# Optimization experiments

Measured on AMD Instinct MI355X. Metric: run time of the kernel, lower is better.

## Reference

```python
import jax, jax.numpy as jnp
import numpy as np

B, NN, HL = 64, 64, 50
IN_DIM, POS_DIM, ATT_DIM = 384, 64, 256
NEWS_DIM = IN_DIM + POS_DIM  # 448


def setup_inputs() -> dict:
    key = jax.random.key(0)
    ks = jax.random.split(key, 8)
    pos_emb = jax.random.uniform(ks[3], (100, POS_DIM), jnp.float32, -0.1, 0.1)
    pos_emb = pos_emb.at[0].set(0.0)  # initialize() zeros row 0
    return {
        "log_vec": jax.random.normal(ks[0], (B, HL, IN_DIM), jnp.float32),
        "log_mask": jax.random.randint(ks[1], (B, HL), 0, 2, jnp.int32),
        "news_vec": jax.random.normal(ks[2], (B, NN, IN_DIM), jnp.float32),
        "pos_emb": pos_emb,
        "W1": jax.random.normal(ks[4], (ATT_DIM, 2 * NEWS_DIM), jnp.float32) * 0.02,
        "b1": jnp.zeros((ATT_DIM,), jnp.float32),
        "W2": jax.random.normal(ks[5], (1, ATT_DIM), jnp.float32) * 0.02,
        "b2": jnp.zeros((1,), jnp.float32),
    }


def reference(log_vec, log_mask, news_vec, pos_emb, W1, b1, W2, b2):
    b, nn_ = news_vec.shape[:2]
    hl = log_mask.shape[1]
    # append position embeddings (row 0 for candidates, rows 1..hl for history)
    nf = jnp.concatenate(
        [news_vec, jnp.broadcast_to(pos_emb[0], (b, nn_, POS_DIM))], axis=-1)   # (B,NN,ND)
    lf = jnp.concatenate(
        [log_vec, jnp.broadcast_to(pos_emb[1:hl + 1], (b, hl, POS_DIM))], axis=-1)  # (B,HL,ND)
    # affine1(cat[news, log]) == news @ Wn^T + log @ Wl^T + b1 (avoids concat)
    Wn, Wl = W1[:, :NEWS_DIM], W1[:, NEWS_DIM:]
    pn = jnp.einsum('bnd,ad->bna', nf, Wn)   # (B,NN,A)
    pl = jnp.einsum('bhd,ad->bha', lf, Wl)   # (B,HL,A)
    h = jnp.tanh(pn[:, :, None, :] + pl[:, None, :, :] + b1)  # (B,NN,HL,A)
    logits = jnp.einsum('bnha,a->bnh', h, W2[0]) + b2[0]      # (B,NN,HL)
    logits = jnp.where(log_mask[:, None, :] == 0, jnp.float32(-1e9), logits)
    attn = jax.nn.softmax(logits, axis=2)
    user_log_vecs = jnp.einsum('bnh,bhd->bnd', attn, lf)      # (B,NN,ND)
    return user_log_vecs, nf
```

## Files before the change

kernel.cpp:

```cpp
#include <hip/hip_runtime.h>
#include <math.h>

typedef unsigned short u16;
typedef unsigned int   u32;

#define B_       64
#define NN_      64
#define HL_      50
#define IN_DIM   384
#define POS_DIM  64
#define ATT_DIM  256
#define NEWS_DIM 448

typedef __attribute__((ext_vector_type(8))) short short8;
typedef __attribute__((ext_vector_type(4))) float f32x4;

#if __has_builtin(__builtin_amdgcn_exp2f)
#define EXP2F(x) __builtin_amdgcn_exp2f(x)
#else
#define EXP2F(x) exp2f(x)
#endif
#if __has_builtin(__builtin_amdgcn_rcpf)
#define RCPF(x) __builtin_amdgcn_rcpf(x)
#else
#define RCPF(x) (1.0f/(x))
#endif

__device__ __forceinline__ u16 f2bf(float f) {
    union { float f; u32 i; } v; v.f = f;
    u32 r = v.i + 0x7fffu + ((v.i >> 16) & 1u);
    return (u16)(r >> 16);
}
__device__ __forceinline__ float bf2f(u16 u) {
    union { u32 i; float f; } v; v.i = ((u32)u) << 16; return v.f;
}
__device__ __forceinline__ uint2 pack4(float4 v) {
    return make_uint2((u32)f2bf(v.x) | ((u32)f2bf(v.y) << 16),
                      (u32)f2bf(v.z) | ((u32)f2bf(v.w) << 16));
}
__device__ __forceinline__ float fast_tanh(float x) {
    float e = EXP2F(x * 2.88539008f);
    return 1.0f - 2.0f * RCPF(1.0f + e);
}

#define C_W   57344u
#define C_NV  393216u
#define C_LG  307200u
#define C_PS  51200u
#define C_NZ  65536u
#define C_TOT (C_W + C_NV + C_LG + C_PS + C_NZ)

__global__ __launch_bounds__(256) void prep_k(
    const float* __restrict__ W1, const float* __restrict__ newsv,
    const float* __restrict__ logv, const float* __restrict__ pos,
    u16* __restrict__ Wbf, u16* __restrict__ nv_bf, u16* __restrict__ lf_bf,
    float* __restrict__ nf)
{
    u32 i = blockIdx.x * 256u + threadIdx.x;
    if (i < C_W) {
        float4 v = *(const float4*)(W1 + (size_t)i * 4u);
        *(uint2*)(Wbf + (size_t)i * 4u) = pack4(v);
        return;
    }
    i -= C_W;
    if (i < C_NV) {
        float4 v = *(const float4*)(newsv + (size_t)i * 4u);
        *(uint2*)(nv_bf + (size_t)i * 4u) = pack4(v);
        u32 e = i * 4u, r = e / IN_DIM, d = e - r * IN_DIM;
        *(float4*)(nf + (size_t)r * NEWS_DIM + d) = v;
        return;
    }
    i -= C_NV;
    if (i < C_LG) {
        float4 v = *(const float4*)(logv + (size_t)i * 4u);
        u32 e = i * 4u, r = e / IN_DIM, d = e - r * IN_DIM;
        *(uint2*)(lf_bf + (size_t)r * NEWS_DIM + d) = pack4(v);
        return;
    }
    i -= C_LG;
    if (i < C_PS) {
        u32 e = i * 4u, r = e / POS_DIM, d = e - r * POS_DIM;
        u32 h = r % HL_;
        float4 v = *(const float4*)(pos + (size_t)(1u + h) * POS_DIM + d);
        *(uint2*)(lf_bf + (size_t)r * NEWS_DIM + IN_DIM + d) = pack4(v);
        return;
    }
    i -= C_PS;
    if (i < C_NZ) {
        u32 e = i * 4u, r = e / POS_DIM, d = e - r * POS_DIM;
        *(float4*)(nf + (size_t)r * NEWS_DIM + IN_DIM + d) = make_float4(0.f, 0.f, 0.f, 0.f);
    }
}

__global__ __launch_bounds__(64) void gemm_k(
    const u16* __restrict__ nv_bf, const u16* __restrict__ lf_bf,
    const u16* __restrict__ Wbf, const float* __restrict__ b1,
    float* __restrict__ pn, float* __restrict__ plT)
{
    int bid = blockIdx.x;
    int lane = threadIdx.x;
    int m = lane & 15, q = lane >> 4;
    bool is_pn = bid < 256;
    int r0, c0, lda, koff, klen;
    const u16* A;
    if (is_pn) { r0 = (bid & 63) * 64;       c0 = (bid >> 6) * 64; A = nv_bf; lda = IN_DIM;   koff = 0;        klen = IN_DIM; }
    else { int b2 = bid - 256; r0 = (b2 % 50) * 64; c0 = (b2 / 50) * 64; A = lf_bf; lda = NEWS_DIM; koff = NEWS_DIM; klen = NEWS_DIM; }

    f32x4 acc[4][4];
#pragma unroll
    for (int a = 0; a < 4; a++)
#pragma unroll
        for (int b = 0; b < 4; b++) acc[a][b] = (f32x4){0.f, 0.f, 0.f, 0.f};

    const u16* Ap = A + (size_t)(r0 + m) * lda + q * 8;
    const u16* Wp = Wbf + (size_t)(c0 + m) * (2 * NEWS_DIM) + koff + q * 8;

    for (int k = 0; k < klen; k += 32) {
        short8 af[4], wf[4];
#pragma unroll
        for (int rt = 0; rt < 4; rt++) af[rt] = *(const short8*)(Ap + rt * 16 * lda + k);
#pragma unroll
        for (int ct = 0; ct < 4; ct++) wf[ct] = *(const short8*)(Wp + ct * 16 * (2 * NEWS_DIM) + k);
#pragma unroll
        for (int rt = 0; rt < 4; rt++)
#pragma unroll
            for (int ct = 0; ct < 4; ct++)
                acc[rt][ct] = __builtin_amdgcn_mfma_f32_16x16x32_bf16(
                    af[rt], wf[ct], acc[rt][ct], 0, 0, 0);
    }
#pragma unroll
    for (int rt = 0; rt < 4; rt++)
#pragma unroll
        for (int ct = 0; ct < 4; ct++)
#pragma unroll
            for (int i = 0; i < 4; i++) {
                int gr = r0 + rt * 16 + q * 4 + i;
                int gc = c0 + ct * 16 + m;
                float v = acc[rt][ct][i];
                if (is_pn) {
                    pn[(size_t)gr * ATT_DIM + gc] = v + b1[gc];
                } else {
                    int bb = gr / HL_, hh = gr - bb * HL_;
                    plT[(size_t)(bb * ATT_DIM + gc) * HL_ + hh] = v;
                }
            }
}

__global__ __launch_bounds__(256) void attn_out_k(
    const float* __restrict__ pn, const float* __restrict__ plT,
    const float* __restrict__ w2, const int* __restrict__ lmask,
    const u16* __restrict__ lf_bf, float* __restrict__ out)
{
    __shared__ float at_s[4][64];
    int lane = threadIdx.x & 63;
    int wid = (int)(threadIdx.x >> 6);
    int g = blockIdx.x * 4 + wid;
    int b = g >> 6;
    int n = g & 63;
    int hl = (lane < HL_) ? lane : (HL_ - 1);
    const float* pr = pn + (size_t)g * ATT_DIM;
    const float* pl = plT + (size_t)b * ATT_DIM * HL_ + hl;

    float a0 = 0.f, a1 = 0.f, a2 = 0.f, a3 = 0.f;
#pragma unroll 4
    for (int a = 0; a < ATT_DIM; a += 4) {
        float4 w4 = *(const float4*)(w2 + a);
        float4 p  = *(const float4*)(pr + a);
        float l0 = pl[(a + 0) * HL_];
        float l1 = pl[(a + 1) * HL_];
        float l2 = pl[(a + 2) * HL_];
        float l3 = pl[(a + 3) * HL_];
        a0 = __builtin_fmaf(fast_tanh(p.x + l0), w4.x, a0);
        a1 = __builtin_fmaf(fast_tanh(p.y + l1), w4.y, a1);
        a2 = __builtin_fmaf(fast_tanh(p.z + l2), w4.z, a2);
        a3 = __builtin_fmaf(fast_tanh(p.w + l3), w4.w, a3);
    }
    float acc = (a0 + a1) + (a2 + a3);
    int mv = (lane < HL_) ? lmask[b * HL_ + lane] : 0;
    float logit = mv ? acc : -1e9f;
    float mx = logit;
#pragma unroll
    for (int o = 32; o > 0; o >>= 1) mx = fmaxf(mx, __shfl_xor(mx, o));
    float e = EXP2F((logit - mx) * 1.44269504f);
    float s = e;
#pragma unroll
    for (int o = 32; o > 0; o >>= 1) s += __shfl_xor(s, o);
    at_s[wid][lane] = e * RCPF(s);

    const u16* lfb = lf_bf + (size_t)b * HL_ * NEWS_DIM + lane;
    float acc7[7];
#pragma unroll
    for (int j = 0; j < 7; j++) acc7[j] = 0.f;
    for (int h = 0; h < HL_; h++) {
        float av = at_s[wid][h];
        const u16* row = lfb + (size_t)h * NEWS_DIM;
#pragma unroll
        for (int j = 0; j < 7; j++)
            acc7[j] = fmaf(av, bf2f(row[64 * j]), acc7[j]);
    }
    float* o0 = out + (size_t)g * NEWS_DIM + lane;
#pragma unroll
    for (int j = 0; j < 7; j++) o0[64 * j] = acc7[j];
}

extern "C" void kernel_launch(void* const* d_in, const int* in_sizes, int n_in,
                              void* d_out, int out_size, void* d_ws, size_t ws_size,
                              hipStream_t stream) {
    const float* logv  = (const float*)d_in[0];
    const int*   lmask = (const int*)d_in[1];
    const float* newsv = (const float*)d_in[2];
    const float* pos   = (const float*)d_in[3];
    const float* W1    = (const float*)d_in[4];
    const float* b1    = (const float*)d_in[5];
    const float* w2    = (const float*)d_in[6];

    float* out = (float*)d_out;
    float* nf  = out + (size_t)B_ * NN_ * NEWS_DIM;

    char* ws = (char*)d_ws;
    u16*   lf_bf = (u16*)(ws + 0);
    u16*   Wbf   = (u16*)(ws + 2867200);
    u16*   nv_bf = (u16*)(ws + 3325952);
    float* pn    = (float*)(ws + 6471680);
    float* plT   = (float*)(ws + 10665984);

    prep_k    <<<C_TOT / 256, 256, 0, stream>>>(W1, newsv, logv, pos,
                                                Wbf, nv_bf, lf_bf, nf);
    gemm_k    <<<456, 64, 0, stream>>>(nv_bf, lf_bf, Wbf, b1, pn, plT);
    attn_out_k<<<1024, 256, 0, stream>>>(pn, plT, w2, lmask, lf_bf, out);
}
```

Measured before the change: 133.2 us.

## Split GEMM into smaller tiles and attention over two waves per query

The GEMM tile shrinks from 64x64 to 16x64 per wave, raising the block count from 456 to 1824 so more of the GPU is busy, at the cost of less A/W reuse per wave. The attention kernel now gives each (b,n) query to two waves. Each wave takes half of the ATT_DIM reduction, the partial logits are combined through shared memory with a block barrier, and the two waves split the 448-wide output (one writes columns 0..255, the other 256..447, with a 64-column overlap that is computed twice but written once). This doubles the wave-level parallelism and shortens the serial tanh loop, but adds a __syncthreads and repeats the softmax and mask work in both waves.

Result: slower. 276.6 us (+107.6%).

```diff
diff --git a/kernel.cpp b/kernel.cpp
--- a/kernel.cpp
+++ b/kernel.cpp
@@ -100,71 +100,67 @@
     int bid = blockIdx.x;
     int lane = threadIdx.x;
     int m = lane & 15, q = lane >> 4;
-    bool is_pn = bid < 256;
+    bool is_pn = bid < 1024;
     int r0, c0, lda, koff, klen;
     const u16* A;
-    if (is_pn) { r0 = (bid & 63) * 64;       c0 = (bid >> 6) * 64; A = nv_bf; lda = IN_DIM;   koff = 0;        klen = IN_DIM; }
-    else { int b2 = bid - 256; r0 = (b2 % 50) * 64; c0 = (b2 / 50) * 64; A = lf_bf; lda = NEWS_DIM; koff = NEWS_DIM; klen = NEWS_DIM; }
-
-    f32x4 acc[4][4];
-#pragma unroll
-    for (int a = 0; a < 4; a++)
-#pragma unroll
-        for (int b = 0; b < 4; b++) acc[a][b] = (f32x4){0.f, 0.f, 0.f, 0.f};
+    if (is_pn) { r0 = (bid >> 2) * 16;  c0 = (bid & 3) * 64; A = nv_bf; lda = IN_DIM;   koff = 0;        klen = IN_DIM; }
+    else { int b2 = bid - 1024; r0 = (b2 >> 2) * 16; c0 = (b2 & 3) * 64; A = lf_bf; lda = NEWS_DIM; koff = NEWS_DIM; klen = NEWS_DIM; }
+
+    f32x4 acc[4];
+#pragma unroll
+    for (int b = 0; b < 4; b++) acc[b] = (f32x4){0.f, 0.f, 0.f, 0.f};
 
     const u16* Ap = A + (size_t)(r0 + m) * lda + q * 8;
     const u16* Wp = Wbf + (size_t)(c0 + m) * (2 * NEWS_DIM) + koff + q * 8;
 
     for (int k = 0; k < klen; k += 32) {
-        short8 af[4], wf[4];
-#pragma unroll
-        for (int rt = 0; rt < 4; rt++) af[rt] = *(const short8*)(Ap + rt * 16 * lda + k);
+        short8 af, wf[4];
+        af = *(const short8*)(Ap + k);
 #pragma unroll
         for (int ct = 0; ct < 4; ct++) wf[ct] = *(const short8*)(Wp + ct * 16 * (2 * NEWS_DIM) + k);
 #pragma unroll
-        for (int rt = 0; rt < 4; rt++)
-#pragma unroll
-            for (int ct = 0; ct < 4; ct++)
-                acc[rt][ct] = __builtin_amdgcn_mfma_f32_16x16x32_bf16(
-                    af[rt], wf[ct], acc[rt][ct], 0, 0, 0);
-    }
-#pragma unroll
-    for (int rt = 0; rt < 4; rt++)
-#pragma unroll
         for (int ct = 0; ct < 4; ct++)
-#pragma unroll
-            for (int i = 0; i < 4; i++) {
-                int gr = r0 + rt * 16 + q * 4 + i;
-                int gc = c0 + ct * 16 + m;
-                float v = acc[rt][ct][i];
-                if (is_pn) {
-                    pn[(size_t)gr * ATT_DIM + gc] = v + b1[gc];
-                } else {
-                    int bb = gr / HL_, hh = gr - bb * HL_;
-                    plT[(size_t)(bb * ATT_DIM + gc) * HL_ + hh] = v;
-                }
+            acc[ct] = __builtin_amdgcn_mfma_f32_16x16x32_bf16(af, wf[ct], acc[ct], 0, 0, 0);
+    }
+#pragma unroll
+    for (int ct = 0; ct < 4; ct++)
+#pragma unroll
+        for (int i = 0; i < 4; i++) {
+            int gr = r0 + q * 4 + i;
+            int gc = c0 + ct * 16 + m;
+            float v = acc[ct][i];
+            if (is_pn) {
+                pn[(size_t)gr * ATT_DIM + gc] = v + b1[gc];
+            } else {
+                int bb = gr / HL_, hh = gr - bb * HL_;
+                plT[(size_t)(bb * ATT_DIM + gc) * HL_ + hh] = v;
             }
-}
-
-__global__ __launch_bounds__(256) void attn_out_k(
+        }
+}
+
+__global__ __launch_bounds__(256, 8) void attn_out_k(
     const float* __restrict__ pn, const float* __restrict__ plT,
     const float* __restrict__ w2, const int* __restrict__ lmask,
     const u16* __restrict__ lf_bf, float* __restrict__ out)
 {
+    __shared__ float part[4][64];
     __shared__ float at_s[4][64];
     int lane = threadIdx.x & 63;
-    int wid = (int)(threadIdx.x >> 6);
-    int g = blockIdx.x * 4 + wid;
+    int wid = __builtin_amdgcn_readfirstlane((int)(threadIdx.x >> 6));
+    int pair = wid >> 1;
+    int half = wid & 1;
+    int g = blockIdx.x * 2 + pair;
     int b = g >> 6;
-    int n = g & 63;
     int hl = (lane < HL_) ? lane : (HL_ - 1);
-    const float* pr = pn + (size_t)g * ATT_DIM;
-    const float* pl = plT + (size_t)b * ATT_DIM * HL_ + hl;
+    int aoff = half * 128;
+    const float* pr = pn + (size_t)g * ATT_DIM + aoff;
+    const float* pl = plT + ((size_t)b * ATT_DIM + aoff) * HL_ + hl;
+    const float* w2o = w2 + aoff;
 
     float a0 = 0.f, a1 = 0.f, a2 = 0.f, a3 = 0.f;
-#pragma unroll 4
-    for (int a = 0; a < ATT_DIM; a += 4) {
-        float4 w4 = *(const float4*)(w2 + a);
+#pragma unroll 2
+    for (int a = 0; a < 128; a += 4) {
+        float4 w4 = *(const float4*)(w2o + a);
         float4 p  = *(const float4*)(pr + a);
         float l0 = pl[(a + 0) * HL_];
         float l1 = pl[(a + 1) * HL_];
@@ -176,6 +172,10 @@
         a3 = __builtin_fmaf(fast_tanh(p.w + l3), w4.w, a3);
     }
     float acc = (a0 + a1) + (a2 + a3);
+    part[wid][lane] = acc;
+    __syncthreads();
+    acc += part[wid ^ 1][lane];
+
     int mv = (lane < HL_) ? lmask[b * HL_ + lane] : 0;
     float logit = mv ? acc : -1e9f;
     float mx = logit;
@@ -187,20 +187,22 @@
     for (int o = 32; o > 0; o >>= 1) s += __shfl_xor(s, o);
     at_s[wid][lane] = e * RCPF(s);
 
-    const u16* lfb = lf_bf + (size_t)b * HL_ * NEWS_DIM + lane;
-    float acc7[7];
-#pragma unroll
-    for (int j = 0; j < 7; j++) acc7[j] = 0.f;
+    const u16* lfb = lf_bf + (size_t)b * HL_ * NEWS_DIM + half * 192 + lane;
+    float acc4[4];
+#pragma unroll
+    for (int j = 0; j < 4; j++) acc4[j] = 0.f;
     for (int h = 0; h < HL_; h++) {
         float av = at_s[wid][h];
         const u16* row = lfb + (size_t)h * NEWS_DIM;
 #pragma unroll
-        for (int j = 0; j < 7; j++)
-            acc7[j] = fmaf(av, bf2f(row[64 * j]), acc7[j]);
-    }
-    float* o0 = out + (size_t)g * NEWS_DIM + lane;
-#pragma unroll
-    for (int j = 0; j < 7; j++) o0[64 * j] = acc7[j];
+        for (int j = 0; j < 4; j++)
+            acc4[j] = fmaf(av, bf2f(row[64 * j]), acc4[j]);
+    }
+    float* o0 = out + (size_t)g * NEWS_DIM + half * 192 + lane;
+#pragma unroll
+    for (int j = 0; j < 4; j++)
+        if (half == 0 || j > 0)
+            o0[64 * j] = acc4[j];
 }
 
 extern "C" void kernel_launch(void* const* d_in, const int* in_sizes, int n_in,
@@ -226,6 +228,6 @@
 
     prep_k    <<<C_TOT / 256, 256, 0, stream>>>(W1, newsv, logv, pos,
                                                 Wbf, nv_bf, lf_bf, nf);
-    gemm_k    <<<456, 64, 0, stream>>>(nv_bf, lf_bf, Wbf, b1, pn, plT);
-    attn_out_k<<<1024, 256, 0, stream>>>(pn, plT, w2, lmask, lf_bf, out);
-}
+    gemm_k    <<<1824, 64, 0, stream>>>(nv_bf, lf_bf, Wbf, b1, pn, plT);
+    attn_out_k<<<2048, 256, 0, stream>>>(pn, plT, w2, lmask, lf_bf, out);
+}
```
